# Performance work log

Hardware: AMD Instinct MI355X
Metric: run time of the kernel (lower is better)

Reference implementation:

```python
import jax, jax.numpy as jnp
import numpy as np
import math

B, LQ, LK, D = 16, 2048, 2048, 64

def setup_inputs() -> dict:
    key = jax.random.key(0)
    kq, kk, kv, kn = jax.random.split(key, 4)
    q = jax.random.normal(kq, (B, LQ, D), dtype=jnp.float32)
    k = jax.random.normal(kk, (B, LK, D), dtype=jnp.float32)
    v = jax.random.normal(kv, (B, LK, D), dtype=jnp.float32)
    # valid lengths in [1, LK] so no row is fully masked
    valid_num = jax.random.randint(kn, (B,), 1, LK + 1, dtype=jnp.int32)
    return {"q": q, "k": k, "v": v, "valid_num": valid_num}

def reference(q, k, v, valid_num):
    d = q.shape[-1]
    # [B, LQ, LK] scores
    scores = jnp.einsum('bqd,bkd->bqk', q, k) / math.sqrt(d)
    # 1D valid_num -> same key mask for every query row (matches repeat_interleave)
    key_pos = jnp.arange(k.shape[1], dtype=valid_num.dtype)  # [LK]
    mask = key_pos[None, None, :] < valid_num[:, None, None]  # [B,1,LK] -> broadcast
    scores = jnp.where(mask, scores, -jnp.inf)
    attn = jax.nn.softmax(scores, axis=-1)
    # dropout p=0.0 -> identity (eval/deterministic reference)
    return jnp.einsum('bqk,bkd->bqd', attn, v)
```

## Files before the change

kernel.cpp:

```cpp
#include <hip/hip_runtime.h>


namespace {

constexpr int NB  = 16;
constexpr int SLQ = 2048;
constexpr int SLK = 2048;
constexpr int DH  = 64;
constexpr int KB  = 64;
constexpr int QB  = 128;

typedef _Float16 half8  __attribute__((ext_vector_type(8)));
typedef _Float16 half4  __attribute__((ext_vector_type(4)));
typedef _Float16 half2t __attribute__((ext_vector_type(2)));
typedef float    f32x4  __attribute__((ext_vector_type(4)));

__device__ inline half2t pkrtz(float a, float b) {
    return __builtin_bit_cast(half2t, __builtin_amdgcn_cvt_pkrtz(a, b));
}

__global__ __launch_bounds__(256)
void prepass(const float* __restrict__ kg, const float* __restrict__ vg,
             const int* __restrict__ vn,
             _Float16* __restrict__ kws, _Float16* __restrict__ vws)
{
    __shared__ _Float16 VT[DH][72];
    const int t  = threadIdx.x;
    const int b  = blockIdx.x >> 5;
    const int kt = blockIdx.x & 31;
    if (kt * KB >= vn[b]) return;
    const size_t tileH = ((size_t)(b << 5) + kt) * 4096;

    {
        const float* kp = kg + ((size_t)b * SLK + (size_t)kt * KB) * DH + t * 16;
        f32x4 a0 = ((const f32x4*)kp)[0], a1 = ((const f32x4*)kp)[1];
        f32x4 a2 = ((const f32x4*)kp)[2], a3 = ((const f32x4*)kp)[3];
        union { half2t h2[4]; uint4 u; } o0, o1;
        o0.h2[0] = pkrtz(a0[0], a0[1]); o0.h2[1] = pkrtz(a0[2], a0[3]);
        o0.h2[2] = pkrtz(a1[0], a1[1]); o0.h2[3] = pkrtz(a1[2], a1[3]);
        o1.h2[0] = pkrtz(a2[0], a2[1]); o1.h2[1] = pkrtz(a2[2], a2[3]);
        o1.h2[2] = pkrtz(a3[0], a3[1]); o1.h2[3] = pkrtz(a3[2], a3[3]);
#pragma unroll
        for (int j = 0; j < 2; ++j) {
            const int n = 2 * t + j;
            const int rr = n >> 3, c = n & 7;
            const int dst = rr * 8 + (c ^ (rr & 7));
            *(uint4*)(kws + tileH + (size_t)dst * 8) = j ? o1.u : o0.u;
        }
    }
    {
        const int kr = t >> 2, d0 = (t & 3) * 16;
        const float* vp = vg + ((size_t)b * SLK + (size_t)kt * KB + kr) * DH + d0;
        f32x4 a0 = ((const f32x4*)vp)[0], a1 = ((const f32x4*)vp)[1];
        f32x4 a2 = ((const f32x4*)vp)[2], a3 = ((const f32x4*)vp)[3];
#pragma unroll
        for (int i = 0; i < 4; ++i) {
            VT[d0 + i][kr]      = (_Float16)a0[i];
            VT[d0 + 4 + i][kr]  = (_Float16)a1[i];
            VT[d0 + 8 + i][kr]  = (_Float16)a2[i];
            VT[d0 + 12 + i][kr] = (_Float16)a3[i];
        }
    }
    __syncthreads();
#pragma unroll
    for (int j = 0; j < 2; ++j) {
        const int n = 2 * t + j;
        const int d = n >> 3, c = n & 7;
        const int dst = d * 8 + (c ^ (d & 7));
        half8 hv = *(const half8*)&VT[d][c * 8];
        *(half8*)(vws + tileH + (size_t)dst * 8) = hv;
    }
}

__global__ __launch_bounds__(256)
void attn_fwd(const float* __restrict__ qg, const _Float16* __restrict__ k16,
              const _Float16* __restrict__ v16, const int* __restrict__ vn,
              _Float16* __restrict__ ws_acc, float* __restrict__ ws_ml,
              int nsplit, int tps)
{
    __shared__ __attribute__((aligned(16))) _Float16 KV[2][8192];

    const int t   = threadIdx.x;
    const int l   = t & 63;
    const int w   = t >> 6;
    const int q15 = l & 15;
    const int g   = l >> 4;
    const int swz = (q15 & 7) << 3;

    const int bid = blockIdx.x;
    int b, qt, s;
    if (nsplit == 8) {
        const int k4 = bid >> 8;
        s  = k4;
        b  = (((bid >> 4) & 15) + k4) & 15;
        qt = bid & 15;
    } else {
        b  = bid & 15;
        qt = bid >> 4;
        s  = 0;
    }

    const int valid = vn[b];
    const int nkt   = (valid + KB - 1) / KB;
    const int kt0   = s * tps;
    if (kt0 >= nkt) return;
    const int kt1   = min(nkt, kt0 + tps);

    const int qrow0 = qt * QB + w * 16 + q15;
    const int qrow1 = qrow0 + 64;

    const float QS = 0.18033688011112042f;

    half8 qf[2][2];
#pragma unroll
    for (int qi = 0; qi < 2; ++qi) {
        const float* qp = qg + ((size_t)b * SLQ + (qi ? qrow1 : qrow0)) * DH;
#pragma unroll
        for (int ss = 0; ss < 2; ++ss) {
            const int d0 = 8 * g + 32 * ss;
            f32x4 x = *(const f32x4*)(qp + d0);
            f32x4 y = *(const f32x4*)(qp + d0 + 4);
            half8 h;
#pragma unroll
            for (int i = 0; i < 4; ++i) {
                h[i]     = (_Float16)(x[i] * QS);
                h[i + 4] = (_Float16)(y[i] * QS);
            }
            qf[qi][ss] = h;
        }
    }

    f32x4 acc0[4], acc1[4];
#pragma unroll
    for (int i = 0; i < 4; ++i) { acc0[i] = f32x4{0.f,0.f,0.f,0.f}; acc1[i] = f32x4{0.f,0.f,0.f,0.f}; }
    float m0 = -1e30f, l0 = 0.f, m1 = -1e30f, l1 = 0.f;

    const _Float16* kbase = k16 + (size_t)(b << 5) * 4096;
    const _Float16* vbase = v16 + (size_t)(b << 5) * 4096;

    uint4 rk0, rk1, rv0, rv1;
#define LOADREGS(KT)                                                         \
    {                                                                        \
        const uint4* kp_ = (const uint4*)(kbase + (size_t)(KT) * 4096);      \
        const uint4* vp_ = (const uint4*)(vbase + (size_t)(KT) * 4096);      \
        rk0 = kp_[t]; rk1 = kp_[t + 256];                                    \
        rv0 = vp_[t]; rv1 = vp_[t + 256];                                    \
    }
#define WRITEKV(CUR)                                                         \
    {                                                                        \
        uint4* kl_ = (uint4*)&KV[CUR][0];                                    \
        uint4* vl_ = (uint4*)&KV[CUR][4096];                                 \
        kl_[t] = rk0; kl_[t + 256] = rk1;                                    \
        vl_[t] = rv0; vl_[t + 256] = rv1;                                    \
    }

    LOADREGS(kt0);
    int cur = 0;

    auto softmax_pack = [&](f32x4 (&st)[4], float& m, float& lsum,
                            f32x4 (&acc)[4], half2t (&pk)[4][2]) {
        float x0 = fmaxf(fmaxf(st[0][0], st[0][1]), fmaxf(st[0][2], st[0][3]));
        float x1 = fmaxf(fmaxf(st[1][0], st[1][1]), fmaxf(st[1][2], st[1][3]));
        float x2 = fmaxf(fmaxf(st[2][0], st[2][1]), fmaxf(st[2][2], st[2][3]));
        float x3 = fmaxf(fmaxf(st[3][0], st[3][1]), fmaxf(st[3][2], st[3][3]));
        float tmax = fmaxf(fmaxf(x0, x1), fmaxf(x2, x3));
        tmax = fmaxf(tmax, __shfl_xor(tmax, 16));
        tmax = fmaxf(tmax, __shfl_xor(tmax, 32));
        if (!__all(tmax - m <= 12.0f)) {
            const float mn = fmaxf(m, tmax);
            const float sc = __builtin_amdgcn_exp2f(m - mn);
            lsum *= sc;
#pragma unroll
            for (int mt = 0; mt < 4; ++mt) acc[mt] *= sc;
            m = mn;
        }
        float p[4][4];
#pragma unroll
        for (int mt = 0; mt < 4; ++mt)
#pragma unroll
            for (int r = 0; r < 4; ++r)
                p[mt][r] = __builtin_amdgcn_exp2f(st[mt][r] - m);
        float s0 = (p[0][0] + p[0][1]) + (p[0][2] + p[0][3]);
        float s1 = (p[1][0] + p[1][1]) + (p[1][2] + p[1][3]);
        float s2 = (p[2][0] + p[2][1]) + (p[2][2] + p[2][3]);
        float s3 = (p[3][0] + p[3][1]) + (p[3][2] + p[3][3]);
        float ps = (s0 + s1) + (s2 + s3);
        ps += __shfl_xor(ps, 16);
        ps += __shfl_xor(ps, 32);
        lsum += ps;
#pragma unroll
        for (int mt = 0; mt < 4; ++mt)
#pragma unroll
            for (int rr = 0; rr < 2; ++rr)
                pk[mt][rr] = pkrtz(p[mt][2 * rr], p[mt][2 * rr + 1]);
    };

    for (int kt = kt0; kt < kt1; ++kt) {
        WRITEKV(cur);
        __syncthreads();
        if (kt + 1 < kt1) LOADREGS(kt + 1);

        const _Float16* Kc = &KV[cur][0];
        const _Float16* Vc = &KV[cur][4096];

        f32x4 st0[4], st1[4];
        __builtin_amdgcn_s_setprio(1);
#pragma unroll
        for (int mt = 0; mt < 4; ++mt) {
            f32x4 c0 = f32x4{0.f,0.f,0.f,0.f}, c1 = f32x4{0.f,0.f,0.f,0.f};
#pragma unroll
            for (int ss = 0; ss < 2; ++ss) {
                half8 a = *(const half8*)&Kc[(16 * mt + q15) * 64 + ((8 * g + 32 * ss) ^ swz)];
                c0 = __builtin_amdgcn_mfma_f32_16x16x32_f16(a, qf[0][ss], c0, 0, 0, 0);
                c1 = __builtin_amdgcn_mfma_f32_16x16x32_f16(a, qf[1][ss], c1, 0, 0, 0);
            }
            st0[mt] = c0; st1[mt] = c1;
        }
        __builtin_amdgcn_s_setprio(0);

        const int krem = valid - kt * KB;
        if (krem < KB) {
#pragma unroll
            for (int mt = 0; mt < 4; ++mt)
#pragma unroll
                for (int r = 0; r < 4; ++r)
                    if (16 * mt + 4 * g + r >= krem) { st0[mt][r] = -1e30f; st1[mt][r] = -1e30f; }
        }

        half2t pk0[4][2], pk1[4][2];
        softmax_pack(st0, m0, l0, acc0, pk0);
        softmax_pack(st1, m1, l1, acc1, pk1);

        __builtin_amdgcn_s_setprio(1);
#pragma unroll
        for (int ss = 0; ss < 2; ++ss) {
            union { half2t h2[4]; half8 v; } bf0, bf1;
            bf0.h2[0] = pk0[2 * ss][0]; bf0.h2[1] = pk0[2 * ss][1];
            bf0.h2[2] = pk0[2 * ss + 1][0]; bf0.h2[3] = pk0[2 * ss + 1][1];
            bf1.h2[0] = pk1[2 * ss][0]; bf1.h2[1] = pk1[2 * ss][1];
            bf1.h2[2] = pk1[2 * ss + 1][0]; bf1.h2[3] = pk1[2 * ss + 1][1];
#pragma unroll
            for (int mt = 0; mt < 4; ++mt) {
                union { half4 h4[2]; half8 v; } af;
                af.h4[0] = *(const half4*)&Vc[(16 * mt + q15) * 64 + ((32 * ss + 4 * g) ^ swz)];
                af.h4[1] = *(const half4*)&Vc[(16 * mt + q15) * 64 + ((32 * ss + 16 + 4 * g) ^ swz)];
                acc0[mt] = __builtin_amdgcn_mfma_f32_16x16x32_f16(af.v, bf0.v, acc0[mt], 0, 0, 0);
                acc1[mt] = __builtin_amdgcn_mfma_f32_16x16x32_f16(af.v, bf1.v, acc1[mt], 0, 0, 0);
            }
        }
        __builtin_amdgcn_s_setprio(0);
        cur ^= 1;
    }
#undef LOADREGS
#undef WRITEKV

#pragma unroll
    for (int qi = 0; qi < 2; ++qi) {
        const float inv = 1.0f / (qi ? l1 : l0);
        const float mm  = qi ? m1 : m0;
        const float ll  = qi ? l1 : l0;
        f32x4* ac = qi ? acc1 : acc0;
        const size_t row = (size_t)b * SLQ + (qi ? qrow1 : qrow0);
        _Float16* wp = ws_acc + ((size_t)s * NB * SLQ + row) * DH;
#pragma unroll
        for (int mt = 0; mt < 4; ++mt) {
            union { half2t h2[2]; uint2 u; } o;
            o.h2[0] = pkrtz(ac[mt][0] * inv, ac[mt][1] * inv);
            o.h2[1] = pkrtz(ac[mt][2] * inv, ac[mt][3] * inv);
            *(uint2*)(wp + 16 * mt + 4 * g) = o.u;
        }
        if (g == 0)
            *(float2*)(ws_ml + ((size_t)s * NB * SLQ + row) * 2) = make_float2(mm, ll);
    }
}

__global__ __launch_bounds__(256)
void attn_combine(const _Float16* __restrict__ ws_acc, const float* __restrict__ ws_ml,
                  const int* __restrict__ vn, float* __restrict__ og,
                  int nsplit, int tps)
{
    const int tid = blockIdx.x * 256 + threadIdx.x;
    const int row = tid >> 2;
    const int dq  = (tid & 3) << 4;
    const int b   = row >> 11;

    const int valid = vn[b];
    const int nkt   = (valid + KB - 1) / KB;
    const int nact  = min(nsplit, (nkt + tps - 1) / tps);

    float M = -1e30f;
    for (int s = 0; s < nact; ++s)
        M = fmaxf(M, ws_ml[((size_t)s * NB * SLQ + row) * 2]);

    float L = 0.f;
    f32x4 o[4];
#pragma unroll
    for (int i = 0; i < 4; ++i) o[i] = f32x4{0.f, 0.f, 0.f, 0.f};

    for (int s = 0; s < nact; ++s) {
        const float2 ml = *(const float2*)(ws_ml + ((size_t)s * NB * SLQ + row) * 2);
        const float wl = __builtin_amdgcn_exp2f(ml.x - M) * ml.y;
        L += wl;
        const _Float16* ap = ws_acc + ((size_t)s * NB * SLQ + row) * DH + dq;
        half8 h0 = ((const half8*)ap)[0];
        half8 h1 = ((const half8*)ap)[1];
#pragma unroll
        for (int r = 0; r < 4; ++r) {
            o[0][r] += wl * (float)h0[r];
            o[1][r] += wl * (float)h0[4 + r];
            o[2][r] += wl * (float)h1[r];
            o[3][r] += wl * (float)h1[4 + r];
        }
    }

    const float inv = 1.0f / L;
    float* op = og + (size_t)row * DH + dq;
#pragma unroll
    for (int i = 0; i < 4; ++i) {
        f32x4 r = o[i] * inv;
        *(f32x4*)(op + 4 * i) = r;
    }
}

}

extern "C" void kernel_launch(void* const* d_in, const int* in_sizes, int n_in,
                              void* d_out, int out_size, void* d_ws, size_t ws_size,
                              hipStream_t stream)
{
    const float* q    = (const float*)d_in[0];
    const float* k    = (const float*)d_in[1];
    const float* v    = (const float*)d_in[2];
    const int*   vnum = (const int*)d_in[3];
    float* out = (float*)d_out;

    const size_t k16H  = (size_t)NB * SLK * DH;
    const size_t v16H  = k16H;
    const size_t rowsH = (size_t)NB * SLQ;

    int nsplit = 8;
    {
        const size_t need8 = (k16H + v16H + (size_t)8 * rowsH * DH) * 2
                           + (size_t)8 * rowsH * 2 * 4;
        if (ws_size < need8) nsplit = 1;
    }
    const int tps = (nsplit == 8) ? 4 : 32;

    _Float16* k16    = (_Float16*)d_ws;
    _Float16* v16t   = k16 + k16H;
    _Float16* ws_acc = v16t + v16H;
    float*    ws_ml  = (float*)(ws_acc + (size_t)nsplit * rowsH * DH);

    prepass<<<dim3(NB * (SLK / KB)), dim3(256), 0, stream>>>(k, v, vnum, k16, v16t);

    dim3 gfwd(nsplit == 8 ? 2048 : 256);
    attn_fwd<<<gfwd, dim3(256), 0, stream>>>(q, k16, v16t, vnum, ws_acc, ws_ml,
                                             nsplit, tps);

    attn_combine<<<dim3((NB * SLQ * 4) / 256), dim3(256), 0, stream>>>(
        ws_acc, ws_ml, vnum, out, nsplit, tps);
}
```

Before: 46.89 us.

## Stage K/V via direct global-to-LDS loads, single buffer, split-K 4

Replaces register-staged double-buffered K/V copies with __builtin_amdgcn_global_load_lds direct DMA into a single LDS buffer, which adds an extra barrier per tile and drops the prefetch overlap. The prepass re-permutes the V tile layout so each lane reads V fragments with one 16-byte LDS load instead of two 8-byte loads. Split-K goes from 8 to 4 with 8 tiles per split, halving the grid and the combine workspace traffic. The nsplit=1 fallback also rotates the batch index per q-tile. The serialized load-then-compute per tile risks exposing global memory latency, relying on occupancy from the halved LDS footprint to hide it.

```diff
diff --git a/kernel.cpp b/kernel.cpp
--- a/kernel.cpp
+++ b/kernel.cpp
@@ -17,6 +17,12 @@
 
 __device__ inline half2t pkrtz(float a, float b) {
     return __builtin_bit_cast(half2t, __builtin_amdgcn_cvt_pkrtz(a, b));
+}
+
+typedef const __attribute__((address_space(1))) void* gas1_t;
+typedef __attribute__((address_space(3))) void* las3_t;
+__device__ __forceinline__ void gld16(const void* g, void* l) {
+    __builtin_amdgcn_global_load_lds((gas1_t)g, (las3_t)l, 16, 0, 0);
 }
 
 __global__ __launch_bounds__(256)
@@ -66,9 +72,13 @@
     for (int j = 0; j < 2; ++j) {
         const int n = 2 * t + j;
         const int d = n >> 3, c = n & 7;
-        const int dst = d * 8 + (c ^ (d & 7));
-        half8 hv = *(const half8*)&VT[d][c * 8];
-        *(half8*)(vws + tileH + (size_t)dst * 8) = hv;
+        const int rsw = (d & 7) << 3;
+        const int pA = 32 * (c >> 2) + 8 * ((2 * c) & 3) + 4 * ((c >> 1) & 1);
+        const int pB = 32 * (c >> 2) + 8 * ((2 * c + 1) & 3) + 4 * ((c >> 1) & 1);
+        half4 hA = *(const half4*)&VT[d][c * 8];
+        half4 hB = *(const half4*)&VT[d][c * 8 + 4];
+        *(half4*)(vws + tileH + (size_t)d * 64 + (pA ^ rsw)) = hA;
+        *(half4*)(vws + tileH + (size_t)d * 64 + (pB ^ rsw)) = hB;
     }
 }
 
@@ -78,7 +88,7 @@
               _Float16* __restrict__ ws_acc, float* __restrict__ ws_ml,
               int nsplit, int tps)
 {
-    __shared__ __attribute__((aligned(16))) _Float16 KV[2][8192];
+    __shared__ __attribute__((aligned(16))) _Float16 KV[8192];
 
     const int t   = threadIdx.x;
     const int l   = t & 63;
@@ -89,14 +99,14 @@
 
     const int bid = blockIdx.x;
     int b, qt, s;
-    if (nsplit == 8) {
-        const int k4 = bid >> 8;
-        s  = k4;
-        b  = (((bid >> 4) & 15) + k4) & 15;
+    if (nsplit == 4) {
+        const int k2 = bid >> 8;
+        s  = k2;
+        b  = (((bid >> 4) & 15) + k2) & 15;
         qt = bid & 15;
     } else {
-        b  = bid & 15;
         qt = bid >> 4;
+        b  = ((bid & 15) + qt) & 15;
         s  = 0;
     }
 
@@ -135,27 +145,21 @@
     for (int i = 0; i < 4; ++i) { acc0[i] = f32x4{0.f,0.f,0.f,0.f}; acc1[i] = f32x4{0.f,0.f,0.f,0.f}; }
     float m0 = -1e30f, l0 = 0.f, m1 = -1e30f, l1 = 0.f;
 
-    const _Float16* kbase = k16 + (size_t)(b << 5) * 4096;
-    const _Float16* vbase = v16 + (size_t)(b << 5) * 4096;
-
-    uint4 rk0, rk1, rv0, rv1;
-#define LOADREGS(KT)                                                         \
-    {                                                                        \
-        const uint4* kp_ = (const uint4*)(kbase + (size_t)(KT) * 4096);      \
-        const uint4* vp_ = (const uint4*)(vbase + (size_t)(KT) * 4096);      \
-        rk0 = kp_[t]; rk1 = kp_[t + 256];                                    \
-        rv0 = vp_[t]; rv1 = vp_[t + 256];                                    \
-    }
-#define WRITEKV(CUR)                                                         \
-    {                                                                        \
-        uint4* kl_ = (uint4*)&KV[CUR][0];                                    \
-        uint4* vl_ = (uint4*)&KV[CUR][4096];                                 \
-        kl_[t] = rk0; kl_[t + 256] = rk1;                                    \
-        vl_[t] = rv0; vl_[t + 256] = rv1;                                    \
-    }
-
-    LOADREGS(kt0);
-    int cur = 0;
+    const char* kbase = (const char*)(k16 + (size_t)(b << 5) * 4096);
+    const char* vbase = (const char*)(v16 + (size_t)(b << 5) * 4096);
+    const int wchunk = w * 128;
+
+#define STAGE(KT)                                                              \
+    {                                                                          \
+        const char* kp_ = kbase + (size_t)(KT) * 8192;                         \
+        const char* vp_ = vbase + (size_t)(KT) * 8192;                         \
+        char* kl_ = (char*)&KV[0];                                             \
+        char* vl_ = (char*)&KV[4096];                                          \
+        gld16(kp_ + (wchunk + l) * 16,       kl_ + wchunk * 16);               \
+        gld16(kp_ + (wchunk + 64 + l) * 16,  kl_ + (wchunk + 64) * 16);        \
+        gld16(vp_ + (wchunk + l) * 16,       vl_ + wchunk * 16);               \
+        gld16(vp_ + (wchunk + 64 + l) * 16,  vl_ + (wchunk + 64) * 16);        \
+    }
 
     auto softmax_pack = [&](f32x4 (&st)[4], float& m, float& lsum,
                             f32x4 (&acc)[4], half2t (&pk)[4][2]) {
@@ -196,12 +200,12 @@
     };
 
     for (int kt = kt0; kt < kt1; ++kt) {
-        WRITEKV(cur);
         __syncthreads();
-        if (kt + 1 < kt1) LOADREGS(kt + 1);
-
-        const _Float16* Kc = &KV[cur][0];
-        const _Float16* Vc = &KV[cur][4096];
+        STAGE(kt);
+        __syncthreads();
+
+        const _Float16* Kc = &KV[0];
+        const _Float16* Vc = &KV[4096];
 
         f32x4 st0[4], st1[4];
         __builtin_amdgcn_s_setprio(1);
@@ -241,24 +245,20 @@
             bf1.h2[2] = pk1[2 * ss + 1][0]; bf1.h2[3] = pk1[2 * ss + 1][1];
 #pragma unroll
             for (int mt = 0; mt < 4; ++mt) {
-                union { half4 h4[2]; half8 v; } af;
-                af.h4[0] = *(const half4*)&Vc[(16 * mt + q15) * 64 + ((32 * ss + 4 * g) ^ swz)];
-                af.h4[1] = *(const half4*)&Vc[(16 * mt + q15) * 64 + ((32 * ss + 16 + 4 * g) ^ swz)];
-                acc0[mt] = __builtin_amdgcn_mfma_f32_16x16x32_f16(af.v, bf0.v, acc0[mt], 0, 0, 0);
-                acc1[mt] = __builtin_amdgcn_mfma_f32_16x16x32_f16(af.v, bf1.v, acc1[mt], 0, 0, 0);
+                half8 af = *(const half8*)&Vc[(16 * mt + q15) * 64 + ((32 * ss + 8 * g) ^ swz)];
+                acc0[mt] = __builtin_amdgcn_mfma_f32_16x16x32_f16(af, bf0.v, acc0[mt], 0, 0, 0);
+                acc1[mt] = __builtin_amdgcn_mfma_f32_16x16x32_f16(af, bf1.v, acc1[mt], 0, 0, 0);
             }
         }
         __builtin_amdgcn_s_setprio(0);
-        cur ^= 1;
-    }
-#undef LOADREGS
-#undef WRITEKV
+    }
+#undef STAGE
 
 #pragma unroll
     for (int qi = 0; qi < 2; ++qi) {
-        const float inv = 1.0f / (qi ? l1 : l0);
+        const float ll  = qi ? l1 : l0;
         const float mm  = qi ? m1 : m0;
-        const float ll  = qi ? l1 : l0;
+        const float inv = 1.0f / ll;
         f32x4* ac = qi ? acc1 : acc0;
         const size_t row = (size_t)b * SLQ + (qi ? qrow1 : qrow0);
         _Float16* wp = ws_acc + ((size_t)s * NB * SLQ + row) * DH;
@@ -338,13 +338,13 @@
     const size_t v16H  = k16H;
     const size_t rowsH = (size_t)NB * SLQ;
 
-    int nsplit = 8;
+    int nsplit = 4;
     {
-        const size_t need8 = (k16H + v16H + (size_t)8 * rowsH * DH) * 2
-                           + (size_t)8 * rowsH * 2 * 4;
-        if (ws_size < need8) nsplit = 1;
-    }
-    const int tps = (nsplit == 8) ? 4 : 32;
+        const size_t need4 = (k16H + v16H + (size_t)4 * rowsH * DH) * 2
+                           + (size_t)4 * rowsH * 2 * 4;
+        if (ws_size < need4) nsplit = 1;
+    }
+    const int tps = (nsplit == 4) ? 8 : 32;
 
     _Float16* k16    = (_Float16*)d_ws;
     _Float16* v16t   = k16 + k16H;
@@ -353,7 +353,7 @@
 
     prepass<<<dim3(NB * (SLK / KB)), dim3(256), 0, stream>>>(k, v, vnum, k16, v16t);
 
-    dim3 gfwd(nsplit == 8 ? 2048 : 256);
+    dim3 gfwd(nsplit == 4 ? 1024 : 256);
     attn_fwd<<<gfwd, dim3(256), 0, stream>>>(q, k16, v16t, vnum, ws_acc, ws_ml,
                                              nsplit, tps);
 
```

New measurement: 45.53 us. 1.03x faster.
